# Kernel optimization log

Hardware: AMD Instinct MI355X
Metric: run time of the kernel (lower is better)

The kernel has to match this reference:

```python
import jax, jax.numpy as jnp
import numpy as np

N_HEADS = 16
HIDDEN = 1024
HEAD_SIZE = HIDDEN // N_HEADS  # 64
BATCH = 2
SEQ_LEN = 2048


def setup_inputs() -> dict:
    key = jax.random.key(0)
    k1, k2, k3 = jax.random.split(key, 3)
    x = jax.random.normal(k1, (BATCH, SEQ_LEN, HIDDEN), dtype=jnp.float32)
    # nn.Linear(hidden, 3*hidden): store weight as [in, out] for x @ W
    W_qkv = jax.random.normal(k2, (HIDDEN, 3 * HIDDEN), dtype=jnp.float32) * (HIDDEN ** -0.5)
    b_qkv = jax.random.normal(k3, (3 * HIDDEN,), dtype=jnp.float32) * 0.02
    return {"x": x, "W_qkv": W_qkv, "b_qkv": b_qkv}


def reference(x, W_qkv, b_qkv):
    B, T, D = x.shape
    nh, hs = N_HEADS, HEAD_SIZE
    scale = hs ** -0.5

    # qkv projection, then the module's exact (unusual) reshape:
    # [B,T,3D] viewed as [3,B,T,hs,nh], permuted to [3,B,nh,T,hs]
    y = x @ W_qkv + b_qkv                      # [B, T, 3D]
    qkv = y.reshape(3, B, T, hs, nh).transpose(0, 1, 4, 2, 3)  # [3,B,nh,T,hs]
    q, k, v = qkv[0], qkv[1], qkv[2]

    # KV-cache scatter with arange index over the full seq is an identity write;
    # cache.transpose(1,2) returns k, v unchanged.

    scores = jnp.einsum('bhtd,bhsd->bhts', q, k) * scale       # [B,nh,T,T]
    causal = jnp.tril(jnp.ones((T, T), dtype=bool))
    scores = jnp.where(causal[None, None], scores, -jnp.inf)
    attn = jax.nn.softmax(scores, axis=-1)
    ctx = jnp.einsum('bhts,bhsd->bhtd', attn, v)               # [B,nh,T,hs]
    # rearrange 'b h t d -> b t (h d)'; note self.o is NOT applied in forward
    return ctx.transpose(0, 2, 1, 3).reshape(B, T, nh * hs)
```

## Files before the change

### kernel.cpp

```cpp
#include <hip/hip_runtime.h>
#include <hip/hip_bf16.h>

typedef __attribute__((ext_vector_type(8))) short s8v;
typedef __attribute__((ext_vector_type(4))) short s4v;
typedef __attribute__((ext_vector_type(4))) float f4v;

__device__ __forceinline__ void g2lds16(const void* g, void* l) {
  __builtin_amdgcn_global_load_lds(
      (__attribute__((address_space(1))) void*)(g),
      (__attribute__((address_space(3))) void*)(l), 16, 0, 0);
}

__device__ __forceinline__ short f2bf(float f) {
  __hip_bfloat16 h = __float2bfloat16(f);
  return *reinterpret_cast<short*>(&h);
}

__global__ void k_prep(const float* __restrict__ x, const float* __restrict__ W,
                       __hip_bfloat16* __restrict__ xb, __hip_bfloat16* __restrict__ Wt) {
  int bx = blockIdx.x;
  if (bx < 4096) {
    int i = (bx * 256 + threadIdx.x) * 4;
    float4 v = *(const float4*)(x + i);
    __hip_bfloat16 o[4] = {__float2bfloat16(v.x), __float2bfloat16(v.y),
                           __float2bfloat16(v.z), __float2bfloat16(v.w)};
    *(uint2*)(xb + i) = *(const uint2*)(o);
  } else {
    __shared__ float tile[32][33];
    int r = bx - 4096;
    int rt = r / 96;
    int ct = r - rt * 96;
    int c0 = ct * 32, r0 = rt * 32;
    int tr = threadIdx.x >> 5, tc = threadIdx.x & 31;
#pragma unroll
    for (int i = 0; i < 32; i += 8)
      tile[tr + i][tc] = W[(size_t)(r0 + tr + i) * 3072 + c0 + tc];
    __syncthreads();
#pragma unroll
    for (int i = 0; i < 32; i += 8)
      Wt[(size_t)(c0 + tr + i) * 1024 + r0 + tc] = __float2bfloat16(tile[tc][tr + i]);
  }
}

__global__ __launch_bounds__(256) void k_gemm(const __hip_bfloat16* __restrict__ A,
                                              const __hip_bfloat16* __restrict__ Bt,
                                              const float* __restrict__ bias,
                                              __hip_bfloat16* __restrict__ Q,
                                              __hip_bfloat16* __restrict__ K,
                                              __hip_bfloat16* __restrict__ Vt) {
  __shared__ __align__(16) __hip_bfloat16 As[2][128 * 32];
  __shared__ __align__(16) __hip_bfloat16 Bs[2][128 * 32];
  const int tid = threadIdx.x;
  const int lane = tid & 63, wave = tid >> 6;
  const int m0 = blockIdx.y * 128, n0 = blockIdx.x * 128;
  const int wm = (wave & 1) * 64, wn = (wave >> 1) * 64;
  const int lrow = lane & 15;
  const int quad = lane >> 4;

  f4v acc[4][4] = {};

  auto stage = [&](int k0, int kb) {
#pragma unroll
    for (int c = 0; c < 2; ++c) {
      int e = c * 2048 + tid * 8;
      int row = e >> 5;
      int slot = (e & 31) >> 3;
      int src = k0 + ((slot ^ ((row >> 1) & 3)) << 3);
      g2lds16(A + (size_t)(m0 + row) * 1024 + src, &As[kb][e]);
      g2lds16(Bt + (size_t)(n0 + row) * 1024 + src, &Bs[kb][e]);
    }
  };

  const int swz = (quad ^ ((lrow >> 1) & 3)) * 8;

  stage(0, 0);
  for (int it = 0; it < 32; ++it) {
    __syncthreads();
    if (it < 31) stage((it + 1) * 32, (it + 1) & 1);
    const __hip_bfloat16* Ab = As[it & 1];
    const __hip_bfloat16* Bb = Bs[it & 1];
    s8v af[4], bfr[4];
#pragma unroll
    for (int mi = 0; mi < 4; ++mi) af[mi] = *(const s8v*)(Ab + (wm + mi * 16 + lrow) * 32 + swz);
#pragma unroll
    for (int ni = 0; ni < 4; ++ni) bfr[ni] = *(const s8v*)(Bb + (wn + ni * 16 + lrow) * 32 + swz);
#pragma unroll
    for (int mi = 0; mi < 4; ++mi)
#pragma unroll
      for (int ni = 0; ni < 4; ++ni)
        acc[mi][ni] = __builtin_amdgcn_mfma_f32_16x16x32_bf16(af[mi], bfr[ni], acc[mi][ni], 0, 0, 0);
  }

  const int cw = n0 + wn;
  const int c10 = cw >> 10;
  const int d0 = (cw & 1023) >> 4;
  const int h = lrow;
  float bv[4];
#pragma unroll
  for (int ni = 0; ni < 4; ++ni) bv[ni] = bias[cw + ni * 16 + lrow];

#pragma unroll
  for (int mi = 0; mi < 4; ++mi) {
    int rbase = m0 + wm + mi * 16 + quad * 4;
#pragma unroll
    for (int reg = 0; reg < 4; ++reg) {
      int rr = rbase + reg;
      int u = 3 * rr + c10;
      int s = u >> 12;
      int b = (u >> 11) & 1;
      int t = u & 2047;
      if (s < 2) {
        __hip_bfloat16* dst = (s == 0) ? Q : K;
        const float qs = (s == 0) ? 0.18033688011112042f : 1.0f;
        s4v pk;
#pragma unroll
        for (int ni = 0; ni < 4; ++ni) pk[ni] = f2bf((acc[mi][ni][reg] + bv[ni]) * qs);
        *(s4v*)(dst + ((size_t)(b * 16 + h) * 2048 + t) * 64 + d0) = pk;
      } else {
#pragma unroll
        for (int ni = 0; ni < 4; ++ni)
          Vt[((size_t)(b * 16 + h) * 64 + d0 + ni) * 2048 + t] =
              __float2bfloat16(acc[mi][ni][reg] + bv[ni]);
      }
    }
  }
}

__global__ __launch_bounds__(256, 4) void k_attn(const __hip_bfloat16* __restrict__ Q,
                                                 const __hip_bfloat16* __restrict__ K,
                                                 const __hip_bfloat16* __restrict__ Vt,
                                                 float* __restrict__ out) {
  __shared__ __align__(16) char lds[2][16384];

  const int tid = threadIdx.x;
  const int lane = tid & 63, w = tid >> 6;
  const int l = lane & 15, q = lane >> 4, lx = l & 7;

  const int bid = blockIdx.x;
  const int xcd = bid & 7;
  const int idx = bid >> 3;
  const int bh = xcd + 8 * (idx & 3);
  const int qb = 31 - (idx >> 2);

  const char* Kb = (const char*)(K + (size_t)bh * 131072);
  const char* Vb = (const char*)(Vt + (size_t)bh * 131072);
  const __hip_bfloat16* Qp = Q + (size_t)bh * 131072 + (size_t)qb * 4096;

  s8v Qf[2];
#pragma unroll
  for (int kh = 0; kh < 2; ++kh)
    Qf[kh] = *(const s8v*)(Qp + (size_t)(w * 16 + l) * 64 + kh * 32 + q * 8);

  f4v O[4] = {};
  float m = -INFINITY, lsum = 0.f;
  const int tg = qb * 64 + w * 16 + l;

  auto stage = [&](int j, char* buf) {
#pragma unroll
    for (int c = 0; c < 4; ++c) {
      int chunk = w * 4 + c;
      int ls = chunk * 64 + lane;
      if (chunk < 8) {
        int row = ls >> 3, kb = ls & 7;
        g2lds16(Kb + (size_t)j * 8192 + row * 128 + ((kb ^ (row & 7)) << 4),
                buf + ls * 16);
      } else {
        int ls2 = ls - 512;
        int d = ls2 >> 3, kb = ls2 & 7;
        g2lds16(Vb + (size_t)d * 4096 + (size_t)j * 128 + ((kb ^ (d & 7)) << 4),
                buf + 8192 + ls2 * 16);
      }
    }
  };

  stage(0, lds[0]);
  __syncthreads();

  for (int j = 0; j <= qb; ++j) {
    const char* Kl = lds[j & 1];
    const char* Vl = Kl + 8192;
    if (j < qb) stage(j + 1, lds[(j + 1) & 1]);

    f4v S[4];
#pragma unroll
    for (int nt = 0; nt < 4; ++nt) {
      const char* rowp = Kl + (nt * 16 + l) * 128;
      s8v k0 = *(const s8v*)(rowp + ((q ^ lx) << 4));
      s8v k1 = *(const s8v*)(rowp + (((4 + q) ^ lx) << 4));
      f4v z = {0.f, 0.f, 0.f, 0.f};
      z = __builtin_amdgcn_mfma_f32_16x16x32_bf16(k0, Qf[0], z, 0, 0, 0);
      z = __builtin_amdgcn_mfma_f32_16x16x32_bf16(k1, Qf[1], z, 0, 0, 0);
      S[nt] = z;
    }

    if (j == qb) {
#pragma unroll
      for (int nt = 0; nt < 4; ++nt)
#pragma unroll
        for (int r = 0; r < 4; ++r)
          if (j * 64 + nt * 16 + q * 4 + r > tg) S[nt][r] = -1e30f;
    }

    float mx = S[0][0];
#pragma unroll
    for (int nt = 0; nt < 4; ++nt)
#pragma unroll
      for (int r = 0; r < 4; ++r) mx = fmaxf(mx, S[nt][r]);
    mx = fmaxf(mx, __shfl_xor(mx, 16));
    mx = fmaxf(mx, __shfl_xor(mx, 32));

    if (!__all(mx - m <= 8.f)) {
      float mn = fmaxf(m, mx);
      float alpha = exp2f(m - mn);
      m = mn;
      lsum *= alpha;
#pragma unroll
      for (int dt = 0; dt < 4; ++dt) O[dt] *= alpha;
    }

    float rs = 0.f;
    s4v Pf[4];
#pragma unroll
    for (int nt = 0; nt < 4; ++nt)
#pragma unroll
      for (int r = 0; r < 4; ++r) {
        float e = exp2f(S[nt][r] - m);
        rs += e;
        Pf[nt][r] = f2bf(e);
      }
    rs += __shfl_xor(rs, 16);
    rs += __shfl_xor(rs, 32);
    lsum += rs;

#pragma unroll
    for (int sc = 0; sc < 4; ++sc) {
      int so = ((sc * 2 + (q >> 1)) ^ lx) * 16 + (q & 1) * 8;
#pragma unroll
      for (int dt = 0; dt < 4; ++dt) {
        s4v vv = *(const s4v*)(Vl + (dt * 16 + l) * 128 + so);
        O[dt] = __builtin_amdgcn_mfma_f32_16x16x16bf16_1k(vv, Pf[sc], O[dt], 0, 0, 0);
      }
    }
    __syncthreads();
  }

  float inv = 1.f / lsum;
  int b = bh >> 4, h = bh & 15;
  float* ob = out + ((size_t)b * 2048 + tg) * 1024 + h * 64;
#pragma unroll
  for (int dt = 0; dt < 4; ++dt) {
    f4v val = O[dt] * inv;
    *(f4v*)(ob + dt * 16 + q * 4) = val;
  }
}

extern "C" void kernel_launch(void* const* d_in, const int* in_sizes, int n_in,
                              void* d_out, int out_size, void* d_ws, size_t ws_size,
                              hipStream_t stream) {
  const float* x = (const float*)d_in[0];
  const float* W = (const float*)d_in[1];
  const float* bias = (const float*)d_in[2];
  float* out = (float*)d_out;

  char* ws = (char*)d_ws;
  __hip_bfloat16* xb = (__hip_bfloat16*)ws;
  __hip_bfloat16* Wt = (__hip_bfloat16*)(ws + 8388608);
  __hip_bfloat16* Qg = (__hip_bfloat16*)(ws + 14680064);
  __hip_bfloat16* Kg = (__hip_bfloat16*)(ws + 23068672);
  __hip_bfloat16* Vt = (__hip_bfloat16*)(ws + 31457280);

  k_prep<<<7168, 256, 0, stream>>>(x, W, xb, Wt);
  k_gemm<<<dim3(24, 32), 256, 0, stream>>>(xb, Wt, bias, Qg, Kg, Vt);
  k_attn<<<1024, 256, 0, stream>>>(Qg, Kg, Vt, out);
}
```

Baseline: 176.1 us.

## Process two adjacent query blocks per attention workgroup to share K/V tiles

Each attention workgroup now handles two consecutive 64-row query blocks, so every K/V tile staged into LDS feeds two sets of MFMA work. This halves the grid and cuts the repeated K/V global-to-LDS traffic and LDS reads per unit of output. In exchange, register pressure roughly doubles (the launch bound drops to 2 waves), the first block does one masked-out extra iteration, and the grid has fewer, longer blocks, which may hurt load balance.

Measured after the change: 185.7 us. +5.5%, slower.

```diff
diff --git a/kernel.cpp b/kernel.cpp
--- a/kernel.cpp
+++ b/kernel.cpp
@@ -126,7 +126,7 @@
   }
 }
 
-__global__ __launch_bounds__(256, 4) void k_attn(const __hip_bfloat16* __restrict__ Q,
+__global__ __launch_bounds__(256, 2) void k_attn(const __hip_bfloat16* __restrict__ Q,
                                                  const __hip_bfloat16* __restrict__ K,
                                                  const __hip_bfloat16* __restrict__ Vt,
                                                  float* __restrict__ out) {
@@ -140,20 +140,26 @@
   const int xcd = bid & 7;
   const int idx = bid >> 3;
   const int bh = xcd + 8 * (idx & 3);
-  const int qb = 31 - (idx >> 2);
+  const int kk = 15 - (idx >> 2);
+  const int qA = 2 * kk, qB = 2 * kk + 1;
 
   const char* Kb = (const char*)(K + (size_t)bh * 131072);
   const char* Vb = (const char*)(Vt + (size_t)bh * 131072);
-  const __hip_bfloat16* Qp = Q + (size_t)bh * 131072 + (size_t)qb * 4096;
-
-  s8v Qf[2];
-#pragma unroll
-  for (int kh = 0; kh < 2; ++kh)
-    Qf[kh] = *(const s8v*)(Qp + (size_t)(w * 16 + l) * 64 + kh * 32 + q * 8);
-
-  f4v O[4] = {};
-  float m = -INFINITY, lsum = 0.f;
-  const int tg = qb * 64 + w * 16 + l;
+  const __hip_bfloat16* QpA = Q + (size_t)bh * 131072 + (size_t)qA * 4096;
+  const __hip_bfloat16* QpB = Q + (size_t)bh * 131072 + (size_t)qB * 4096;
+
+  s8v QfA[2], QfB[2];
+#pragma unroll
+  for (int kh = 0; kh < 2; ++kh) {
+    QfA[kh] = *(const s8v*)(QpA + (size_t)(w * 16 + l) * 64 + kh * 32 + q * 8);
+    QfB[kh] = *(const s8v*)(QpB + (size_t)(w * 16 + l) * 64 + kh * 32 + q * 8);
+  }
+
+  f4v OA[4] = {}, OB[4] = {};
+  float mA = -INFINITY, lsA = 0.f;
+  float mB = -INFINITY, lsB = 0.f;
+  const int tgA = qA * 64 + w * 16 + l;
+  const int tgB = qB * 64 + w * 16 + l;
 
   auto stage = [&](int j, char* buf) {
 #pragma unroll
@@ -176,61 +182,91 @@
   stage(0, lds[0]);
   __syncthreads();
 
-  for (int j = 0; j <= qb; ++j) {
+  for (int j = 0; j <= qB; ++j) {
     const char* Kl = lds[j & 1];
     const char* Vl = Kl + 8192;
-    if (j < qb) stage(j + 1, lds[(j + 1) & 1]);
-
-    f4v S[4];
+    if (j < qB) stage(j + 1, lds[(j + 1) & 1]);
+
+    f4v SA[4], SB[4];
 #pragma unroll
     for (int nt = 0; nt < 4; ++nt) {
       const char* rowp = Kl + (nt * 16 + l) * 128;
       s8v k0 = *(const s8v*)(rowp + ((q ^ lx) << 4));
       s8v k1 = *(const s8v*)(rowp + (((4 + q) ^ lx) << 4));
-      f4v z = {0.f, 0.f, 0.f, 0.f};
-      z = __builtin_amdgcn_mfma_f32_16x16x32_bf16(k0, Qf[0], z, 0, 0, 0);
-      z = __builtin_amdgcn_mfma_f32_16x16x32_bf16(k1, Qf[1], z, 0, 0, 0);
-      S[nt] = z;
-    }
-
-    if (j == qb) {
+      f4v zA = {0.f, 0.f, 0.f, 0.f};
+      zA = __builtin_amdgcn_mfma_f32_16x16x32_bf16(k0, QfA[0], zA, 0, 0, 0);
+      zA = __builtin_amdgcn_mfma_f32_16x16x32_bf16(k1, QfA[1], zA, 0, 0, 0);
+      f4v zB = {0.f, 0.f, 0.f, 0.f};
+      zB = __builtin_amdgcn_mfma_f32_16x16x32_bf16(k0, QfB[0], zB, 0, 0, 0);
+      zB = __builtin_amdgcn_mfma_f32_16x16x32_bf16(k1, QfB[1], zB, 0, 0, 0);
+      SA[nt] = zA;
+      SB[nt] = zB;
+    }
+
+    if (j >= qA) {
 #pragma unroll
       for (int nt = 0; nt < 4; ++nt)
 #pragma unroll
         for (int r = 0; r < 4; ++r)
-          if (j * 64 + nt * 16 + q * 4 + r > tg) S[nt][r] = -1e30f;
-    }
-
-    float mx = S[0][0];
+          if (j * 64 + nt * 16 + q * 4 + r > tgA) SA[nt][r] = -1e30f;
+    }
+    if (j == qB) {
+#pragma unroll
+      for (int nt = 0; nt < 4; ++nt)
+#pragma unroll
+        for (int r = 0; r < 4; ++r)
+          if (j * 64 + nt * 16 + q * 4 + r > tgB) SB[nt][r] = -1e30f;
+    }
+
+    float mxA = SA[0][0], mxB = SB[0][0];
 #pragma unroll
     for (int nt = 0; nt < 4; ++nt)
 #pragma unroll
-      for (int r = 0; r < 4; ++r) mx = fmaxf(mx, S[nt][r]);
-    mx = fmaxf(mx, __shfl_xor(mx, 16));
-    mx = fmaxf(mx, __shfl_xor(mx, 32));
-
-    if (!__all(mx - m <= 8.f)) {
-      float mn = fmaxf(m, mx);
-      float alpha = exp2f(m - mn);
-      m = mn;
-      lsum *= alpha;
-#pragma unroll
-      for (int dt = 0; dt < 4; ++dt) O[dt] *= alpha;
-    }
-
-    float rs = 0.f;
-    s4v Pf[4];
+      for (int r = 0; r < 4; ++r) {
+        mxA = fmaxf(mxA, SA[nt][r]);
+        mxB = fmaxf(mxB, SB[nt][r]);
+      }
+    mxA = fmaxf(mxA, __shfl_xor(mxA, 16));
+    mxB = fmaxf(mxB, __shfl_xor(mxB, 16));
+    mxA = fmaxf(mxA, __shfl_xor(mxA, 32));
+    mxB = fmaxf(mxB, __shfl_xor(mxB, 32));
+
+    if (!__all(mxA - mA <= 8.f)) {
+      float mn = fmaxf(mA, mxA);
+      float alpha = exp2f(mA - mn);
+      mA = mn;
+      lsA *= alpha;
+#pragma unroll
+      for (int dt = 0; dt < 4; ++dt) OA[dt] *= alpha;
+    }
+    if (!__all(mxB - mB <= 8.f)) {
+      float mn = fmaxf(mB, mxB);
+      float alpha = exp2f(mB - mn);
+      mB = mn;
+      lsB *= alpha;
+#pragma unroll
+      for (int dt = 0; dt < 4; ++dt) OB[dt] *= alpha;
+    }
+
+    float rsA = 0.f, rsB = 0.f;
+    s4v PfA[4], PfB[4];
 #pragma unroll
     for (int nt = 0; nt < 4; ++nt)
 #pragma unroll
       for (int r = 0; r < 4; ++r) {
-        float e = exp2f(S[nt][r] - m);
-        rs += e;
-        Pf[nt][r] = f2bf(e);
-      }
-    rs += __shfl_xor(rs, 16);
-    rs += __shfl_xor(rs, 32);
-    lsum += rs;
+        float eA = exp2f(SA[nt][r] - mA);
+        float eB = exp2f(SB[nt][r] - mB);
+        rsA += eA;
+        rsB += eB;
+        PfA[nt][r] = f2bf(eA);
+        PfB[nt][r] = f2bf(eB);
+      }
+    rsA += __shfl_xor(rsA, 16);
+    rsB += __shfl_xor(rsB, 16);
+    rsA += __shfl_xor(rsA, 32);
+    rsB += __shfl_xor(rsB, 32);
+    lsA += rsA;
+    lsB += rsB;
 
 #pragma unroll
     for (int sc = 0; sc < 4; ++sc) {
@@ -238,19 +274,23 @@
 #pragma unroll
       for (int dt = 0; dt < 4; ++dt) {
         s4v vv = *(const s4v*)(Vl + (dt * 16 + l) * 128 + so);
-        O[dt] = __builtin_amdgcn_mfma_f32_16x16x16bf16_1k(vv, Pf[sc], O[dt], 0, 0, 0);
+        OA[dt] = __builtin_amdgcn_mfma_f32_16x16x16bf16_1k(vv, PfA[sc], OA[dt], 0, 0, 0);
+        OB[dt] = __builtin_amdgcn_mfma_f32_16x16x16bf16_1k(vv, PfB[sc], OB[dt], 0, 0, 0);
       }
     }
     __syncthreads();
   }
 
-  float inv = 1.f / lsum;
+  float invA = 1.f / lsA, invB = 1.f / lsB;
   int b = bh >> 4, h = bh & 15;
-  float* ob = out + ((size_t)b * 2048 + tg) * 1024 + h * 64;
+  float* obA = out + ((size_t)b * 2048 + tgA) * 1024 + h * 64;
+  float* obB = out + ((size_t)b * 2048 + tgB) * 1024 + h * 64;
 #pragma unroll
   for (int dt = 0; dt < 4; ++dt) {
-    f4v val = O[dt] * inv;
-    *(f4v*)(ob + dt * 16 + q * 4) = val;
+    f4v vA = OA[dt] * invA;
+    f4v vB = OB[dt] * invB;
+    *(f4v*)(obA + dt * 16 + q * 4) = vA;
+    *(f4v*)(obB + dt * 16 + q * 4) = vB;
   }
 }
 
@@ -271,5 +311,5 @@
 
   k_prep<<<7168, 256, 0, stream>>>(x, W, xb, Wt);
   k_gemm<<<dim3(24, 32), 256, 0, stream>>>(xb, Wt, bias, Qg, Kg, Vt);
-  k_attn<<<1024, 256, 0, stream>>>(Qg, Kg, Vt, out);
-}
+  k_attn<<<512, 256, 0, stream>>>(Qg, Kg, Vt, out);
+}
```
